# Kernel optimization log

Measured on AMD Instinct MI355X. Metric: run time of the kernel, lower is better.

## Reference

```python
import jax, jax.numpy as jnp
import numpy as np

V, E, H = 32000, 512, 1024  # vocab, embedding, hidden
B, T = 16, 256


def setup_inputs() -> dict:
    key = jax.random.key(0)
    ks = jax.random.split(key, 7)
    x = jax.random.randint(ks[0], (B, T), 0, V)
    emb = jax.random.normal(ks[1], (V, E), dtype=jnp.float32) * 0.02
    # Keras LSTMCell params: kernel [E,4H], recurrent_kernel [H,4H], bias [4H]
    kernel = jax.random.normal(ks[2], (E, 4 * H), dtype=jnp.float32) * (1.0 / np.sqrt(E))
    rec_kernel = jax.random.normal(ks[3], (H, 4 * H), dtype=jnp.float32) * (1.0 / np.sqrt(H))
    # unit_forget_bias: forget-gate bias initialized to 1 (gate order i,f,c,o)
    bias = jnp.concatenate([jnp.zeros(H), jnp.ones(H), jnp.zeros(2 * H)]).astype(jnp.float32)
    w_out = jax.random.normal(ks[4], (H, V), dtype=jnp.float32) * (1.0 / np.sqrt(H))
    b_out = jnp.zeros((V,), dtype=jnp.float32)
    return {"x": x, "emb": emb, "kernel": kernel, "rec_kernel": rec_kernel,
            "bias": bias, "w_out": w_out, "b_out": b_out}


def _lstm_scan(e, kernel, rec_kernel, bias):
    # e: [B, T, E] -> h_seq [B, T, H]
    Bsz = e.shape[0]
    Hs = rec_kernel.shape[0]
    # Precompute input projections for all timesteps (one big GEMM)
    zx = jnp.einsum('bte,ef->btf', e, kernel) + bias  # [B, T, 4H]
    zx_t = jnp.transpose(zx, (1, 0, 2))  # [T, B, 4H]

    def step(carry, zxt):
        h, c = carry
        z = zxt + h @ rec_kernel  # [B, 4H]
        i, f, g, o = jnp.split(z, 4, axis=-1)  # Keras gate order: i, f, c(g), o
        i = jax.nn.sigmoid(i)
        f = jax.nn.sigmoid(f)
        g = jnp.tanh(g)
        o = jax.nn.sigmoid(o)
        c = f * c + i * g
        h = o * jnp.tanh(c)
        return (h, c), h

    h0 = jnp.zeros((Bsz, Hs), dtype=e.dtype)
    c0 = jnp.zeros((Bsz, Hs), dtype=e.dtype)
    _, h_seq = jax.lax.scan(step, (h0, c0), zx_t)  # [T, B, H]
    return jnp.transpose(h_seq, (1, 0, 2))  # [B, T, H]


def reference(x, emb, kernel, rec_kernel, bias, w_out, b_out):
    e = emb[x]  # [B, T, E] embedding lookup
    h = _lstm_scan(e, kernel, rec_kernel, bias)  # [B, T, H]
    logits = jnp.einsum('bth,hv->btv', h, w_out) + b_out  # [B, T, V]
    return logits
```

## Files before the change

### kernel.cpp

```cpp
#include <hip/hip_runtime.h>
#include <cstdint>
#include <cstddef>

#define DEV __device__ __forceinline__

typedef __attribute__((ext_vector_type(4))) float f32x4;
typedef __attribute__((ext_vector_type(8))) short s16x8;
typedef __attribute__((ext_vector_type(4))) unsigned u32x4;

DEV uint16_t f2bf(float x){
  union { float f; uint32_t u; } v; v.f = x;
  uint32_t r = v.u + 0x7FFFu + ((v.u >> 16) & 1u);
  return (uint16_t)(r >> 16);
}
DEV float bf2f(uint16_t h){
  union { uint32_t u; float f; } v; v.u = ((uint32_t)h) << 16; return v.f;
}
DEV void split2(float x, uint16_t &hi, uint16_t &lo){
  hi = f2bf(x); lo = f2bf(x - bf2f(hi));
}

DEV f32x4 mfma16(s16x8 a, s16x8 b, f32x4 c){
  return __builtin_amdgcn_mfma_f32_16x16x32_bf16(a, b, c, 0, 0, 0);
}

DEV void g2l16(const void* g, void* l){
  __builtin_amdgcn_global_load_lds(
      (const __attribute__((address_space(1))) unsigned int*)g,
      (__attribute__((address_space(3))) unsigned int*)l, 16, 0, 0);
}

DEV s16x8 ldg_coh(const uint16_t* p){
  s16x8 r;
  asm volatile("global_load_dwordx4 %0, %1, off sc0 sc1" : "=v"(r) : "v"(p));
  return r;
}
DEV void stg_coh64(uint16_t* p, unsigned long long v){
  asm volatile("global_store_dwordx2 %0, %1, off sc0 sc1"
               :: "v"(p), "v"(v) : "memory");
}
DEV void stg_coh32(unsigned* p, unsigned v){
  asm volatile("global_store_dword %0, %1, off sc0 sc1"
               :: "v"(p), "v"(v) : "memory");
}
DEV u32x4 ldg_coh_u4(const unsigned* p){
  u32x4 r;
  asm volatile("global_load_dwordx4 %0, %1, off sc0 sc1\n\t"
               "s_waitcnt vmcnt(0)"
               : "=v"(r) : "v"(p) : "memory");
  return r;
}

__global__ void zero_u32(unsigned* __restrict__ p){ p[threadIdx.x] = 0u; }

__global__ __launch_bounds__(256) void gather_split(
    const int* __restrict__ x, const float* __restrict__ emb,
    uint16_t* __restrict__ ehi, uint16_t* __restrict__ elo){
  int idx = blockIdx.x * 256 + threadIdx.x;
  int r = idx >> 7, k4 = idx & 127;
  int row = x[r];
  float4 v = ((const float4*)(emb + (size_t)row * 512))[k4];
  ushort4 hi, lo;
  split2(v.x, hi.x, lo.x);
  split2(v.y, hi.y, lo.y);
  split2(v.z, hi.z, lo.z);
  split2(v.w, hi.w, lo.w);
  ((ushort4*)ehi)[idx] = hi;
  ((ushort4*)elo)[idx] = lo;
}

__global__ __launch_bounds__(256) void transpose_split(
    const float* __restrict__ in, uint16_t* __restrict__ ohi,
    uint16_t* __restrict__ olo, int R, int Cc){
  __shared__ float tile[32][33];
  const int tx = threadIdx.x & 31, ty = threadIdx.x >> 5;
  const int c0 = blockIdx.x << 5, r0 = blockIdx.y << 5;
  for (int i = 0; i < 32; i += 8)
    tile[ty + i][tx] = in[(size_t)(r0 + ty + i) * Cc + c0 + tx];
  __syncthreads();
  for (int i = 0; i < 32; i += 8){
    float v = tile[tx][ty + i];
    uint16_t hi, lo; split2(v, hi, lo);
    size_t o = (size_t)(c0 + ty + i) * R + r0 + tx;
    ohi[o] = hi; olo[o] = lo;
  }
}

__global__ __launch_bounds__(256) void pack_wr(
    const float* __restrict__ wr, uint16_t* __restrict__ phi, uint16_t* __restrict__ plo){
  int t = blockIdx.x * 256 + threadIdx.x;
  int lane = t & 63, kb = (t >> 6) & 31, ntile = t >> 11;
  int q = lane >> 4, ln = lane & 15;
  int n = ((ln >> 2) << 10) + (ntile << 2) + (ln & 3);
  int k0 = (kb << 5) + (q << 3);
  union { s16x8 v; uint16_t e[8]; } uh, ul;
  for (int j = 0; j < 8; j++)
    split2(wr[(size_t)(k0 + j) * 4096 + n], uh.e[j], ul.e[j]);
  ((s16x8*)phi)[t] = uh.v;
  ((s16x8*)plo)[t] = ul.v;
}

__global__ __launch_bounds__(256) void gemm_split(
    const uint16_t* __restrict__ Ahi, const uint16_t* __restrict__ Alo,
    const uint16_t* __restrict__ Bhi, const uint16_t* __restrict__ Blo,
    const float* __restrict__ bias, float* __restrict__ C,
    int Mm, int Nn, int Kk){
  __shared__ __attribute__((aligned(16))) uint16_t sAhi[2][128 * 32];
  __shared__ __attribute__((aligned(16))) uint16_t sAlo[2][128 * 32];
  __shared__ __attribute__((aligned(16))) uint16_t sBhi[2][128 * 32];
  __shared__ __attribute__((aligned(16))) uint16_t sBlo[2][128 * 32];

  const int tid = threadIdx.x;
  const int lane = tid & 63, wid = tid >> 6;
  const int wm = (wid & 1) * 64, wn = (wid >> 1) * 64;
  const int q = lane >> 4, lm = lane & 15;

  const int gm = Mm >> 7, gn = Nn >> 7;
  const int GROUP = 10;
  const int per = gm * GROUP;
  const int gi = blockIdx.x / per;
  const int rem = blockIdx.x - gi * per;
  const int n0g = gi * GROUP;
  int gw = gn - n0g; if (gw > GROUP) gw = GROUP;
  const int mt = rem / gw;
  const int nt = n0g + rem % gw;
  const int m0 = mt << 7, n0 = nt << 7;

  const int row0 = tid >> 2;
  const int csw  = (tid & 3) ^ ((row0 + (row0 >> 2)) & 3);
  const size_t aoff0 = (size_t)(m0 + row0) * Kk + csw * 8;
  const size_t aoff1 = (size_t)(m0 + row0 + 64) * Kk + csw * 8;
  const size_t boff0 = (size_t)(n0 + row0) * Kk + csw * 8;
  const size_t boff1 = (size_t)(n0 + row0 + 64) * Kk + csw * 8;

  const int qs8 = ((q ^ ((lm + (lm >> 2)) & 3)) * 8);

  auto STAGE = [&](int b, int ks){
    g2l16(Ahi + aoff0 + ks, sAhi[b] + tid * 8);
    g2l16(Ahi + aoff1 + ks, sAhi[b] + 2048 + tid * 8);
    g2l16(Alo + aoff0 + ks, sAlo[b] + tid * 8);
    g2l16(Alo + aoff1 + ks, sAlo[b] + 2048 + tid * 8);
    g2l16(Bhi + boff0 + ks, sBhi[b] + tid * 8);
    g2l16(Bhi + boff1 + ks, sBhi[b] + 2048 + tid * 8);
    g2l16(Blo + boff0 + ks, sBlo[b] + tid * 8);
    g2l16(Blo + boff1 + ks, sBlo[b] + 2048 + tid * 8);
  };

  f32x4 acc[4][4];
  for (int i = 0; i < 4; i++) for (int j = 0; j < 4; j++)
    acc[i][j] = (f32x4){0.f, 0.f, 0.f, 0.f};

  STAGE(0, 0);
  __syncthreads();

  int buf = 0;
  for (int ks = 0; ks < Kk; ks += 32){
    if (ks + 32 < Kk) STAGE(buf ^ 1, ks + 32);

    const uint16_t* pAh = sAhi[buf];
    const uint16_t* pAl = sAlo[buf];
    const uint16_t* pBh = sBhi[buf];
    const uint16_t* pBl = sBlo[buf];

    s16x8 bh[4], bl[4];
    for (int j = 0; j < 4; j++){
      bh[j] = *(const s16x8*)&pBh[(wn + j * 16 + lm) * 32 + qs8];
      bl[j] = *(const s16x8*)&pBl[(wn + j * 16 + lm) * 32 + qs8];
    }
    for (int i = 0; i < 4; i++){
      s16x8 ah = *(const s16x8*)&pAh[(wm + i * 16 + lm) * 32 + qs8];
      s16x8 al = *(const s16x8*)&pAl[(wm + i * 16 + lm) * 32 + qs8];
      for (int j = 0; j < 4; j++){
        acc[i][j] = mfma16(ah, bh[j], acc[i][j]);
        acc[i][j] = mfma16(ah, bl[j], acc[i][j]);
        acc[i][j] = mfma16(al, bh[j], acc[i][j]);
      }
    }
    __syncthreads();
    buf ^= 1;
  }

  for (int i = 0; i < 4; i++){
    const int rowg = m0 + wm + i * 16 + q * 4;
    for (int j = 0; j < 4; j++){
      const int colg = n0 + wn + j * 16 + lm;
      const float bv = bias[colg];
      for (int r = 0; r < 4; r++)
        C[(size_t)(rowg + r) * Nn + colg] = acc[i][j][r] + bv;
    }
  }
}

__global__ __launch_bounds__(256, 2) void lstm_fused(
    const uint16_t* __restrict__ wphi, const uint16_t* __restrict__ wplo,
    const float* __restrict__ zx,
    uint16_t* __restrict__ hseq_hi, uint16_t* __restrict__ hseq_lo,
    uint16_t* __restrict__ h0hi, uint16_t* __restrict__ h0lo,
    uint16_t* __restrict__ h1hi, uint16_t* __restrict__ h1lo,
    unsigned* __restrict__ flags, unsigned* __restrict__ epoch){
  __shared__ __attribute__((aligned(16))) uint16_t sWh[32 * 64 * 8];
  __shared__ __attribute__((aligned(16))) uint16_t sWl[32 * 64 * 8];
  __shared__ float zbuf[4][16][17];

  const int tid = threadIdx.x, lane = tid & 63, w = tid >> 6;
  const int q = lane >> 4, lm = lane & 15;
  const int blk = blockIdx.x;
  const int kq = w;
  const bool is_master = (blk == 0 && w == 0);

  {
    const uint16_t* gh = wphi + (size_t)blk * 16384;
    const uint16_t* gl = wplo + (size_t)blk * 16384;
#pragma unroll
    for (int i = 0; i < 8; i++){
      const int o = (i * 256 + tid) * 8;
      g2l16(gh + o, sWh + o);
      g2l16(gl + o, sWl + o);
    }
    asm volatile("s_waitcnt vmcnt(0)" ::: "memory");
  }
  __syncthreads();

  const int aoffbase = lm * 1024 + kq * 256 + q * 8;
  const int boffbase = kq * 8 * 512 + lane * 8;

  const int tb = tid >> 2, ccin = tid & 3;
  const int thcol = blk * 4 + ccin;
  const unsigned* epoll = epoch + (blk & 7) * 32;
  float cval = 0.f;

  for (int t = 0; t < 256; t++){
    float zr0 = 0.f, zr1 = 0.f, zr2 = 0.f, zr3 = 0.f;
    if (tid < 64){
      const float* zr = zx + ((size_t)tb * 256 + t) * 4096 + thcol;
      zr0 = zr[0]; zr1 = zr[1024]; zr2 = zr[2048]; zr3 = zr[3072];
    }

    f32x4 a0 = (f32x4){0.f,0.f,0.f,0.f};
    f32x4 a1 = (f32x4){0.f,0.f,0.f,0.f};
    f32x4 a2 = (f32x4){0.f,0.f,0.f,0.f};
    if (t > 0){
      if (!is_master){
        const unsigned gen = (unsigned)t;
        for (;;){
          unsigned v;
          asm volatile("global_load_dword %0, %1, off sc0 sc1\n\t"
                       "s_waitcnt vmcnt(0)"
                       : "=v"(v) : "v"(epoll) : "memory");
          if (v >= gen) break;
          __builtin_amdgcn_s_sleep(1);
        }
      }
      __builtin_amdgcn_sched_barrier(0);

      const uint16_t* hih = (t & 1) ? h1hi : h0hi;
      const uint16_t* hil = (t & 1) ? h1lo : h0lo;
      const uint16_t* ah_p = hih + aoffbase;
      const uint16_t* al_p = hil + aoffbase;
      s16x8 Ah[8], Al[8];
#pragma unroll
      for (int kb = 0; kb < 8; kb++){
        Ah[kb] = ldg_coh(ah_p + kb * 32);
        Al[kb] = ldg_coh(al_p + kb * 32);
      }
      asm volatile("s_waitcnt vmcnt(0)" ::: "memory");
      __builtin_amdgcn_sched_barrier(0);
#pragma unroll
      for (int kb = 0; kb < 8; kb++){
        s16x8 bh = *(const s16x8*)&sWh[boffbase + kb * 512];
        s16x8 bl = *(const s16x8*)&sWl[boffbase + kb * 512];
        a0 = mfma16(Ah[kb], bh, a0);
        a1 = mfma16(Ah[kb], bl, a1);
        a2 = mfma16(Al[kb], bh, a2);
      }
    }
    f32x4 acc = a0 + a1 + a2;

#pragma unroll
    for (int r = 0; r < 4; r++)
      zbuf[w][q * 4 + r][lm] = acc[r];
    __syncthreads();

    if (tid < 64){
      const size_t rrow = (size_t)tb * 256 + t;
      float z0 = zbuf[0][tb][0 * 4 + ccin] + zbuf[1][tb][0 * 4 + ccin]
               + zbuf[2][tb][0 * 4 + ccin] + zbuf[3][tb][0 * 4 + ccin] + zr0;
      float z1 = zbuf[0][tb][1 * 4 + ccin] + zbuf[1][tb][1 * 4 + ccin]
               + zbuf[2][tb][1 * 4 + ccin] + zbuf[3][tb][1 * 4 + ccin] + zr1;
      float z2 = zbuf[0][tb][2 * 4 + ccin] + zbuf[1][tb][2 * 4 + ccin]
               + zbuf[2][tb][2 * 4 + ccin] + zbuf[3][tb][2 * 4 + ccin] + zr2;
      float z3 = zbuf[0][tb][3 * 4 + ccin] + zbuf[1][tb][3 * 4 + ccin]
               + zbuf[2][tb][3 * 4 + ccin] + zbuf[3][tb][3 * 4 + ccin] + zr3;
      float ig = 1.f / (1.f + __expf(-z0));
      float fg = 1.f / (1.f + __expf(-z1));
      float gg = 1.f - 2.f / (__expf(2.f * z2) + 1.f);
      float og = 1.f / (1.f + __expf(-z3));
      cval = fg * cval + ig * gg;
      float h = og * (1.f - 2.f / (__expf(2.f * cval) + 1.f));
      uint16_t hh, hl; split2(h, hh, hl);

      unsigned pk = (unsigned)hh | ((unsigned)hl << 16);
      unsigned p1 = __shfl_down(pk, 1);
      unsigned p2 = __shfl_down(pk, 2);
      unsigned p3 = __shfl_down(pk, 3);
      if (ccin == 0){
        union { unsigned u32[2]; unsigned long long u64; } vhi, vlo;
        vhi.u32[0] = (pk & 0xFFFFu) | ((p1 & 0xFFFFu) << 16);
        vhi.u32[1] = (p2 & 0xFFFFu) | ((p3 & 0xFFFFu) << 16);
        vlo.u32[0] = (pk >> 16) | (p1 & 0xFFFF0000u);
        vlo.u32[1] = (p2 >> 16) | (p3 & 0xFFFF0000u);
        uint16_t* ohh = ((t & 1) ? h0hi : h1hi) + tb * 1024 + blk * 4;
        uint16_t* ohl = ((t & 1) ? h0lo : h1lo) + tb * 1024 + blk * 4;
        stg_coh64(ohh, vhi.u64);
        stg_coh64(ohl, vlo.u64);
      }
      asm volatile("s_waitcnt vmcnt(0)" ::: "memory");
      if (tid == 0)
        stg_coh32(flags + blk, (unsigned)(t + 1));
      hseq_hi[rrow * 1024 + thcol] = hh;
      hseq_lo[rrow * 1024 + thcol] = hl;
    }

    if (is_master && t < 255){
      const unsigned gen = (unsigned)(t + 1);
      for (;;){
        u32x4 f = ldg_coh_u4(flags + lane * 4);
        if (__all(f.x >= gen && f.y >= gen && f.z >= gen && f.w >= gen)) break;
        __builtin_amdgcn_s_sleep(1);
      }
      if (lane < 8)
        stg_coh32(epoch + lane * 32, gen);
    }
  }
}

extern "C" void kernel_launch(void* const* d_in, const int* in_sizes, int n_in,
                              void* d_out, int out_size, void* d_ws, size_t ws_size,
                              hipStream_t stream){
  (void)in_sizes; (void)n_in; (void)out_size; (void)ws_size;
  const int*   x    = (const int*)d_in[0];
  const float* emb  = (const float*)d_in[1];
  const float* wk   = (const float*)d_in[2];
  const float* wr   = (const float*)d_in[3];
  const float* bias = (const float*)d_in[4];
  const float* wo   = (const float*)d_in[5];
  const float* bo   = (const float*)d_in[6];
  float* out = (float*)d_out;

  char* w = (char*)d_ws;
  float*    zx    = (float*)w;    w += (size_t)4096 * 4096 * 4;
  uint16_t* ehi   = (uint16_t*)w; w += (size_t)4096 * 512 * 2;
  uint16_t* elo   = (uint16_t*)w; w += (size_t)4096 * 512 * 2;
  uint16_t* kthi  = (uint16_t*)w; w += (size_t)4096 * 512 * 2;
  uint16_t* ktlo  = (uint16_t*)w; w += (size_t)4096 * 512 * 2;
  uint16_t* wphi  = (uint16_t*)w; w += (size_t)1024 * 4096 * 2;
  uint16_t* wplo  = (uint16_t*)w; w += (size_t)1024 * 4096 * 2;
  uint16_t* wothi = (uint16_t*)w; w += (size_t)32000 * 1024 * 2;
  uint16_t* wotlo = (uint16_t*)w; w += (size_t)32000 * 1024 * 2;
  uint16_t* hshi  = (uint16_t*)w; w += (size_t)4096 * 1024 * 2;
  uint16_t* hslo  = (uint16_t*)w; w += (size_t)4096 * 1024 * 2;
  uint16_t* h0hi  = (uint16_t*)w; w += (size_t)16 * 1024 * 2;
  uint16_t* h0lo  = (uint16_t*)w; w += (size_t)16 * 1024 * 2;
  uint16_t* h1hi  = (uint16_t*)w; w += (size_t)16 * 1024 * 2;
  uint16_t* h1lo  = (uint16_t*)w; w += (size_t)16 * 1024 * 2;
  unsigned* flags = (unsigned*)w; w += 256 * 4;
  unsigned* epoch = (unsigned*)w; w += 256 * 4;

  zero_u32<<<1, 512, 0, stream>>>(flags);
  gather_split<<<2048, 256, 0, stream>>>(x, emb, ehi, elo);
  transpose_split<<<dim3(128, 16), 256, 0, stream>>>(wk, kthi, ktlo, 512, 4096);
  pack_wr<<<2048, 256, 0, stream>>>(wr, wphi, wplo);
  transpose_split<<<dim3(1000, 32), 256, 0, stream>>>(wo, wothi, wotlo, 1024, 32000);

  gemm_split<<<1024, 256, 0, stream>>>(ehi, elo, kthi, ktlo, bias, zx,
                                       4096, 4096, 512);

  {
    void* kargs[] = {
      (void*)&wphi, (void*)&wplo, (void*)&zx,
      (void*)&hshi, (void*)&hslo,
      (void*)&h0hi, (void*)&h0lo, (void*)&h1hi, (void*)&h1lo,
      (void*)&flags, (void*)&epoch
    };
    (void)hipLaunchCooperativeKernel((void*)lstm_fused, dim3(256), dim3(256),
                                     kargs, 0, stream);
  }

  gemm_split<<<8000, 256, 0, stream>>>(hshi, hslo, wothi, wotlo, bo, out,
                                       4096, 32000, 1024);
}
```

Measured before the change: 2.818 ms.

## Enlarge split-bf16 GEMM tiles to 256x256 with 8 waves and explicit pipelining

The split-precision GEMM goes from 128x128 tiles with 4 waves to 256x256 tiles with 512 threads. Each wave now computes a 128x64 sub-tile. The K loop prefetches two stages ahead using explicit vmcnt waits, raw s_barrier calls and setprio around the MFMA phases. The aim is to raise arithmetic intensity and keep MFMA units busy in the large output-projection GEMM. In exchange it uses much more LDS and registers, runs one block per CU, and leaves fewer blocks for the small input-projection GEMM.

New measurement: 2.874 ms. 1.02x slower.

```diff
diff --git a/kernel.cpp b/kernel.cpp
--- a/kernel.cpp
+++ b/kernel.cpp
@@ -100,23 +100,23 @@
   ((s16x8*)plo)[t] = ul.v;
 }
 
-__global__ __launch_bounds__(256) void gemm_split(
+__global__ __launch_bounds__(512, 1) void gemm_split(
     const uint16_t* __restrict__ Ahi, const uint16_t* __restrict__ Alo,
     const uint16_t* __restrict__ Bhi, const uint16_t* __restrict__ Blo,
     const float* __restrict__ bias, float* __restrict__ C,
     int Mm, int Nn, int Kk){
-  __shared__ __attribute__((aligned(16))) uint16_t sAhi[2][128 * 32];
-  __shared__ __attribute__((aligned(16))) uint16_t sAlo[2][128 * 32];
-  __shared__ __attribute__((aligned(16))) uint16_t sBhi[2][128 * 32];
-  __shared__ __attribute__((aligned(16))) uint16_t sBlo[2][128 * 32];
+  __shared__ __attribute__((aligned(16))) uint16_t sAh[2][8192];
+  __shared__ __attribute__((aligned(16))) uint16_t sAl[2][8192];
+  __shared__ __attribute__((aligned(16))) uint16_t sBh[2][8192];
+  __shared__ __attribute__((aligned(16))) uint16_t sBl[2][8192];
 
   const int tid = threadIdx.x;
   const int lane = tid & 63, wid = tid >> 6;
-  const int wm = (wid & 1) * 64, wn = (wid >> 1) * 64;
+  const int wm = (wid & 1) * 128, wn = (wid >> 1) * 64;
   const int q = lane >> 4, lm = lane & 15;
 
-  const int gm = Mm >> 7, gn = Nn >> 7;
-  const int GROUP = 10;
+  const int gm = Mm >> 8, gn = Nn >> 8;
+  const int GROUP = 8;
   const int per = gm * GROUP;
   const int gi = blockIdx.x / per;
   const int rem = blockIdx.x - gi * per;
@@ -124,63 +124,89 @@
   int gw = gn - n0g; if (gw > GROUP) gw = GROUP;
   const int mt = rem / gw;
   const int nt = n0g + rem % gw;
-  const int m0 = mt << 7, n0 = nt << 7;
+  const int m0 = mt << 8, n0 = nt << 8;
 
   const int row0 = tid >> 2;
   const int csw  = (tid & 3) ^ ((row0 + (row0 >> 2)) & 3);
-  const size_t aoff0 = (size_t)(m0 + row0) * Kk + csw * 8;
-  const size_t aoff1 = (size_t)(m0 + row0 + 64) * Kk + csw * 8;
-  const size_t boff0 = (size_t)(n0 + row0) * Kk + csw * 8;
-  const size_t boff1 = (size_t)(n0 + row0 + 64) * Kk + csw * 8;
+  const size_t aoffA0 = (size_t)(m0 + row0) * Kk + csw * 8;
+  const size_t aoffA1 = (size_t)(m0 + row0 + 128) * Kk + csw * 8;
+  const size_t aoffB0 = (size_t)(n0 + row0) * Kk + csw * 8;
+  const size_t aoffB1 = (size_t)(n0 + row0 + 128) * Kk + csw * 8;
 
   const int qs8 = ((q ^ ((lm + (lm >> 2)) & 3)) * 8);
 
   auto STAGE = [&](int b, int ks){
-    g2l16(Ahi + aoff0 + ks, sAhi[b] + tid * 8);
-    g2l16(Ahi + aoff1 + ks, sAhi[b] + 2048 + tid * 8);
-    g2l16(Alo + aoff0 + ks, sAlo[b] + tid * 8);
-    g2l16(Alo + aoff1 + ks, sAlo[b] + 2048 + tid * 8);
-    g2l16(Bhi + boff0 + ks, sBhi[b] + tid * 8);
-    g2l16(Bhi + boff1 + ks, sBhi[b] + 2048 + tid * 8);
-    g2l16(Blo + boff0 + ks, sBlo[b] + tid * 8);
-    g2l16(Blo + boff1 + ks, sBlo[b] + 2048 + tid * 8);
+    g2l16(Ahi + aoffA0 + ks, &sAh[b][tid * 8]);
+    g2l16(Ahi + aoffA1 + ks, &sAh[b][(tid + 512) * 8]);
+    g2l16(Alo + aoffA0 + ks, &sAl[b][tid * 8]);
+    g2l16(Alo + aoffA1 + ks, &sAl[b][(tid + 512) * 8]);
+    g2l16(Bhi + aoffB0 + ks, &sBh[b][tid * 8]);
+    g2l16(Bhi + aoffB1 + ks, &sBh[b][(tid + 512) * 8]);
+    g2l16(Blo + aoffB0 + ks, &sBl[b][tid * 8]);
+    g2l16(Blo + aoffB1 + ks, &sBl[b][(tid + 512) * 8]);
   };
 
-  f32x4 acc[4][4];
-  for (int i = 0; i < 4; i++) for (int j = 0; j < 4; j++)
-    acc[i][j] = (f32x4){0.f, 0.f, 0.f, 0.f};
-
+  f32x4 acc[8][4];
+#pragma unroll
+  for (int i = 0; i < 8; i++)
+#pragma unroll
+    for (int j = 0; j < 4; j++)
+      acc[i][j] = (f32x4){0.f, 0.f, 0.f, 0.f};
+
+  const int ns = Kk >> 5;
   STAGE(0, 0);
-  __syncthreads();
-
-  int buf = 0;
-  for (int ks = 0; ks < Kk; ks += 32){
-    if (ks + 32 < Kk) STAGE(buf ^ 1, ks + 32);
-
-    const uint16_t* pAh = sAhi[buf];
-    const uint16_t* pAl = sAlo[buf];
-    const uint16_t* pBh = sBhi[buf];
-    const uint16_t* pBl = sBlo[buf];
-
-    s16x8 bh[4], bl[4];
-    for (int j = 0; j < 4; j++){
-      bh[j] = *(const s16x8*)&pBh[(wn + j * 16 + lm) * 32 + qs8];
-      bl[j] = *(const s16x8*)&pBl[(wn + j * 16 + lm) * 32 + qs8];
-    }
-    for (int i = 0; i < 4; i++){
-      s16x8 ah = *(const s16x8*)&pAh[(wm + i * 16 + lm) * 32 + qs8];
-      s16x8 al = *(const s16x8*)&pAl[(wm + i * 16 + lm) * 32 + qs8];
-      for (int j = 0; j < 4; j++){
-        acc[i][j] = mfma16(ah, bh[j], acc[i][j]);
-        acc[i][j] = mfma16(ah, bl[j], acc[i][j]);
-        acc[i][j] = mfma16(al, bh[j], acc[i][j]);
-      }
-    }
-    __syncthreads();
-    buf ^= 1;
-  }
-
-  for (int i = 0; i < 4; i++){
+  if (ns > 1) STAGE(1, 32);
+
+  for (int it = 0; it < ns; ++it){
+    const int ks = it << 5;
+    const int buf = it & 1;
+
+    if (it + 1 < ns) asm volatile("s_waitcnt vmcnt(8)" ::: "memory");
+    else             asm volatile("s_waitcnt vmcnt(0)" ::: "memory");
+    __builtin_amdgcn_sched_barrier(0);
+    __builtin_amdgcn_s_barrier();
+    __builtin_amdgcn_sched_barrier(0);
+
+#pragma unroll
+    for (int ph = 0; ph < 4; ++ph){
+      const int mq = ph & 1, nq = ph >> 1;
+      s16x8 ah[4], al[4], bh[2], bl[2];
+#pragma unroll
+      for (int ii = 0; ii < 4; ii++){
+        const int row = wm + (mq * 4 + ii) * 16 + lm;
+        ah[ii] = *(const s16x8*)&sAh[buf][row * 32 + qs8];
+        al[ii] = *(const s16x8*)&sAl[buf][row * 32 + qs8];
+      }
+#pragma unroll
+      for (int jj = 0; jj < 2; jj++){
+        const int row = wn + (nq * 2 + jj) * 16 + lm;
+        bh[jj] = *(const s16x8*)&sBh[buf][row * 32 + qs8];
+        bl[jj] = *(const s16x8*)&sBl[buf][row * 32 + qs8];
+      }
+      if (ph == 3){
+        asm volatile("s_waitcnt lgkmcnt(0)" ::: "memory");
+        __builtin_amdgcn_sched_barrier(0);
+        __builtin_amdgcn_s_barrier();
+        if (ks + 64 < Kk) STAGE(buf, ks + 64);
+      }
+      __builtin_amdgcn_s_setprio(1);
+#pragma unroll
+      for (int ii = 0; ii < 4; ii++){
+        const int ai = mq * 4 + ii;
+#pragma unroll
+        for (int jj = 0; jj < 2; jj++){
+          const int bj = nq * 2 + jj;
+          acc[ai][bj] = mfma16(ah[ii], bh[jj], acc[ai][bj]);
+          acc[ai][bj] = mfma16(ah[ii], bl[jj], acc[ai][bj]);
+          acc[ai][bj] = mfma16(al[ii], bh[jj], acc[ai][bj]);
+        }
+      }
+      __builtin_amdgcn_s_setprio(0);
+      __builtin_amdgcn_s_barrier();
+    }
+  }
+
+  for (int i = 0; i < 8; i++){
     const int rowg = m0 + wm + i * 16 + q * 4;
     for (int j = 0; j < 4; j++){
       const int colg = n0 + wn + j * 16 + lm;
@@ -372,8 +398,8 @@
   pack_wr<<<2048, 256, 0, stream>>>(wr, wphi, wplo);
   transpose_split<<<dim3(1000, 32), 256, 0, stream>>>(wo, wothi, wotlo, 1024, 32000);
 
-  gemm_split<<<1024, 256, 0, stream>>>(ehi, elo, kthi, ktlo, bias, zx,
-                                       4096, 4096, 512);
+  gemm_split<<<256, 512, 0, stream>>>(ehi, elo, kthi, ktlo, bias, zx,
+                                      4096, 4096, 512);
 
   {
     void* kargs[] = {
@@ -386,6 +412,6 @@
                                      kargs, 0, stream);
   }
 
-  gemm_split<<<8000, 256, 0, stream>>>(hshi, hslo, wothi, wotlo, bo, out,
+  gemm_split<<<2000, 512, 0, stream>>>(hshi, hslo, wothi, wotlo, bo, out,
                                        4096, 32000, 1024);
 }
```

## Overlap output projection GEMM with LSTM recurrence in one cooperative kernel

Applied to the files above, without the earlier changes.

Launches 512 cooperative blocks. The first 256 run the LSTM recurrence, and the rest compute output-logit GEMM tiles as soon as the epoch counter shows the needed timesteps are finished. Hidden states are written in time-major (rotated) order so that each 128-row tile covers 8 complete timesteps, and the epilogue permutes rows back to batch-major order. This hides the large vocab GEMM behind the latency-bound recurrence. The cost is that the GEMM blocks share the GPU with the recurrence blocks and may slow its critical path. A fallback to separate launches is kept in case the 512-block cooperative launch fails.

Result: faster. 2.300 ms (-18.4%).

```diff
diff --git a/kernel.cpp b/kernel.cpp
--- a/kernel.cpp
+++ b/kernel.cpp
@@ -49,6 +49,13 @@
                "s_waitcnt vmcnt(0)"
                : "=v"(r) : "v"(p) : "memory");
   return r;
+}
+DEV unsigned ldg_coh_u1(const unsigned* p){
+  unsigned v;
+  asm volatile("global_load_dword %0, %1, off sc0 sc1\n\t"
+               "s_waitcnt vmcnt(0)"
+               : "=v"(v) : "v"(p) : "memory");
+  return v;
 }
 
 __global__ void zero_u32(unsigned* __restrict__ p){ p[threadIdx.x] = 0u; }
@@ -104,7 +111,7 @@
     const uint16_t* __restrict__ Ahi, const uint16_t* __restrict__ Alo,
     const uint16_t* __restrict__ Bhi, const uint16_t* __restrict__ Blo,
     const float* __restrict__ bias, float* __restrict__ C,
-    int Mm, int Nn, int Kk){
+    int Mm, int Nn, int Kk, int rowperm){
   __shared__ __attribute__((aligned(16))) uint16_t sAhi[2][128 * 32];
   __shared__ __attribute__((aligned(16))) uint16_t sAlo[2][128 * 32];
   __shared__ __attribute__((aligned(16))) uint16_t sBhi[2][128 * 32];
@@ -185,26 +192,132 @@
     for (int j = 0; j < 4; j++){
       const int colg = n0 + wn + j * 16 + lm;
       const float bv = bias[colg];
-      for (int r = 0; r < 4; r++)
-        C[(size_t)(rowg + r) * Nn + colg] = acc[i][j][r] + bv;
-    }
-  }
-}
+      for (int r = 0; r < 4; r++){
+        int rg = rowg + r;
+        if (rowperm) rg = ((rg & 15) << 8) | (rg >> 4);
+        C[(size_t)rg * Nn + colg] = acc[i][j][r] + bv;
+      }
+    }
+  }
+}
+
+struct SMemRec {
+  uint16_t Wh[32 * 64 * 8];
+  uint16_t Wl[32 * 64 * 8];
+  float zbuf[4][16][17];
+};
+struct SMemGw {
+  uint16_t Ah[2][4096];
+  uint16_t Al[2][4096];
+  uint16_t Bh[2][4096];
+  uint16_t Bl[2][4096];
+};
+union SMemU { SMemRec rec; SMemGw gw; };
 
 __global__ __launch_bounds__(256, 2) void lstm_fused(
     const uint16_t* __restrict__ wphi, const uint16_t* __restrict__ wplo,
     const float* __restrict__ zx,
-    uint16_t* __restrict__ hseq_hi, uint16_t* __restrict__ hseq_lo,
+    uint16_t* __restrict__ hrot_hi, uint16_t* __restrict__ hrot_lo,
     uint16_t* __restrict__ h0hi, uint16_t* __restrict__ h0lo,
     uint16_t* __restrict__ h1hi, uint16_t* __restrict__ h1lo,
-    unsigned* __restrict__ flags, unsigned* __restrict__ epoch){
-  __shared__ __attribute__((aligned(16))) uint16_t sWh[32 * 64 * 8];
-  __shared__ __attribute__((aligned(16))) uint16_t sWl[32 * 64 * 8];
-  __shared__ float zbuf[4][16][17];
+    unsigned* __restrict__ flags, unsigned* __restrict__ epoch,
+    const uint16_t* __restrict__ wothi, const uint16_t* __restrict__ wotlo,
+    const float* __restrict__ bo, float* __restrict__ out){
+  __shared__ __attribute__((aligned(16))) SMemU sm;
 
   const int tid = threadIdx.x, lane = tid & 63, w = tid >> 6;
+  const int blk = blockIdx.x;
+
+  if (blk >= 256){
+    const int wb = blk - 256;
+    const int wid = tid >> 6;
+    const int wm = (wid & 1) * 64, wn = (wid >> 1) * 64;
+    const int q = lane >> 4, lm = lane & 15;
+    const int row0 = tid >> 2;
+    const int csw = (tid & 3) ^ ((row0 + (row0 >> 2)) & 3);
+    const int qs8 = ((q ^ ((lm + (lm >> 2)) & 3)) * 8);
+    const unsigned* ep = epoch + (wb & 7) * 32;
+
+    for (int idx = wb; idx < 8000; idx += 256){
+      const int mt = idx / 250, nt = idx - mt * 250;
+      const unsigned need = (unsigned)(mt * 8 + 8);
+      for (;;){
+        if (ldg_coh_u1(ep) >= need) break;
+        __builtin_amdgcn_s_sleep(2);
+      }
+      __builtin_amdgcn_sched_barrier(0);
+
+      const int m0 = mt << 7, n0 = nt << 7;
+      const size_t aoff0 = (size_t)(m0 + row0) * 1024 + csw * 8;
+      const size_t aoff1 = (size_t)(m0 + row0 + 64) * 1024 + csw * 8;
+      const size_t boff0 = (size_t)(n0 + row0) * 1024 + csw * 8;
+      const size_t boff1 = (size_t)(n0 + row0 + 64) * 1024 + csw * 8;
+
+      auto STAGEW = [&](int b, int ks){
+        g2l16(hrot_hi + aoff0 + ks, &sm.gw.Ah[b][tid * 8]);
+        g2l16(hrot_hi + aoff1 + ks, &sm.gw.Ah[b][2048 + tid * 8]);
+        g2l16(hrot_lo + aoff0 + ks, &sm.gw.Al[b][tid * 8]);
+        g2l16(hrot_lo + aoff1 + ks, &sm.gw.Al[b][2048 + tid * 8]);
+        g2l16(wothi + boff0 + ks, &sm.gw.Bh[b][tid * 8]);
+        g2l16(wothi + boff1 + ks, &sm.gw.Bh[b][2048 + tid * 8]);
+        g2l16(wotlo + boff0 + ks, &sm.gw.Bl[b][tid * 8]);
+        g2l16(wotlo + boff1 + ks, &sm.gw.Bl[b][2048 + tid * 8]);
+      };
+
+      f32x4 acc[4][4];
+#pragma unroll
+      for (int i = 0; i < 4; i++)
+#pragma unroll
+        for (int j = 0; j < 4; j++)
+          acc[i][j] = (f32x4){0.f, 0.f, 0.f, 0.f};
+
+      STAGEW(0, 0);
+      __syncthreads();
+      int buf = 0;
+      for (int ks = 0; ks < 1024; ks += 32){
+        if (ks + 32 < 1024) STAGEW(buf ^ 1, ks + 32);
+        const uint16_t* pAh = sm.gw.Ah[buf];
+        const uint16_t* pAl = sm.gw.Al[buf];
+        const uint16_t* pBh = sm.gw.Bh[buf];
+        const uint16_t* pBl = sm.gw.Bl[buf];
+        s16x8 bh[4], bl[4];
+#pragma unroll
+        for (int j = 0; j < 4; j++){
+          bh[j] = *(const s16x8*)&pBh[(wn + j * 16 + lm) * 32 + qs8];
+          bl[j] = *(const s16x8*)&pBl[(wn + j * 16 + lm) * 32 + qs8];
+        }
+#pragma unroll
+        for (int i = 0; i < 4; i++){
+          s16x8 ah = *(const s16x8*)&pAh[(wm + i * 16 + lm) * 32 + qs8];
+          s16x8 al = *(const s16x8*)&pAl[(wm + i * 16 + lm) * 32 + qs8];
+#pragma unroll
+          for (int j = 0; j < 4; j++){
+            acc[i][j] = mfma16(ah, bh[j], acc[i][j]);
+            acc[i][j] = mfma16(ah, bl[j], acc[i][j]);
+            acc[i][j] = mfma16(al, bh[j], acc[i][j]);
+          }
+        }
+        __syncthreads();
+        buf ^= 1;
+      }
+
+      for (int i = 0; i < 4; i++){
+        const int rowg = m0 + wm + i * 16 + q * 4;
+        for (int j = 0; j < 4; j++){
+          const int colg = n0 + wn + j * 16 + lm;
+          const float bv = bo[colg];
+          for (int r = 0; r < 4; r++){
+            int rg = rowg + r;
+            rg = ((rg & 15) << 8) | (rg >> 4);
+            out[(size_t)rg * 32000 + colg] = acc[i][j][r] + bv;
+          }
+        }
+      }
+    }
+    return;
+  }
+
   const int q = lane >> 4, lm = lane & 15;
-  const int blk = blockIdx.x;
   const int kq = w;
   const bool is_master = (blk == 0 && w == 0);
 
@@ -214,8 +327,8 @@
 #pragma unroll
     for (int i = 0; i < 8; i++){
       const int o = (i * 256 + tid) * 8;
-      g2l16(gh + o, sWh + o);
-      g2l16(gl + o, sWl + o);
+      g2l16(gh + o, sm.rec.Wh + o);
+      g2l16(gl + o, sm.rec.Wl + o);
     }
     asm volatile("s_waitcnt vmcnt(0)" ::: "memory");
   }
@@ -243,11 +356,7 @@
       if (!is_master){
         const unsigned gen = (unsigned)t;
         for (;;){
-          unsigned v;
-          asm volatile("global_load_dword %0, %1, off sc0 sc1\n\t"
-                       "s_waitcnt vmcnt(0)"
-                       : "=v"(v) : "v"(epoll) : "memory");
-          if (v >= gen) break;
+          if (ldg_coh_u1(epoll) >= gen) break;
           __builtin_amdgcn_s_sleep(1);
         }
       }
@@ -267,8 +376,8 @@
       __builtin_amdgcn_sched_barrier(0);
 #pragma unroll
       for (int kb = 0; kb < 8; kb++){
-        s16x8 bh = *(const s16x8*)&sWh[boffbase + kb * 512];
-        s16x8 bl = *(const s16x8*)&sWl[boffbase + kb * 512];
+        s16x8 bh = *(const s16x8*)&sm.rec.Wh[boffbase + kb * 512];
+        s16x8 bl = *(const s16x8*)&sm.rec.Wl[boffbase + kb * 512];
         a0 = mfma16(Ah[kb], bh, a0);
         a1 = mfma16(Ah[kb], bl, a1);
         a2 = mfma16(Al[kb], bh, a2);
@@ -278,19 +387,18 @@
 
 #pragma unroll
     for (int r = 0; r < 4; r++)
-      zbuf[w][q * 4 + r][lm] = acc[r];
+      sm.rec.zbuf[w][q * 4 + r][lm] = acc[r];
     __syncthreads();
 
     if (tid < 64){
-      const size_t rrow = (size_t)tb * 256 + t;
-      float z0 = zbuf[0][tb][0 * 4 + ccin] + zbuf[1][tb][0 * 4 + ccin]
-               + zbuf[2][tb][0 * 4 + ccin] + zbuf[3][tb][0 * 4 + ccin] + zr0;
-      float z1 = zbuf[0][tb][1 * 4 + ccin] + zbuf[1][tb][1 * 4 + ccin]
-               + zbuf[2][tb][1 * 4 + ccin] + zbuf[3][tb][1 * 4 + ccin] + zr1;
-      float z2 = zbuf[0][tb][2 * 4 + ccin] + zbuf[1][tb][2 * 4 + ccin]
-               + zbuf[2][tb][2 * 4 + ccin] + zbuf[3][tb][2 * 4 + ccin] + zr2;
-      float z3 = zbuf[0][tb][3 * 4 + ccin] + zbuf[1][tb][3 * 4 + ccin]
-               + zbuf[2][tb][3 * 4 + ccin] + zbuf[3][tb][3 * 4 + ccin] + zr3;
+      float z0 = sm.rec.zbuf[0][tb][0 * 4 + ccin] + sm.rec.zbuf[1][tb][0 * 4 + ccin]
+               + sm.rec.zbuf[2][tb][0 * 4 + ccin] + sm.rec.zbuf[3][tb][0 * 4 + ccin] + zr0;
+      float z1 = sm.rec.zbuf[0][tb][1 * 4 + ccin] + sm.rec.zbuf[1][tb][1 * 4 + ccin]
+               + sm.rec.zbuf[2][tb][1 * 4 + ccin] + sm.rec.zbuf[3][tb][1 * 4 + ccin] + zr1;
+      float z2 = sm.rec.zbuf[0][tb][2 * 4 + ccin] + sm.rec.zbuf[1][tb][2 * 4 + ccin]
+               + sm.rec.zbuf[2][tb][2 * 4 + ccin] + sm.rec.zbuf[3][tb][2 * 4 + ccin] + zr2;
+      float z3 = sm.rec.zbuf[0][tb][3 * 4 + ccin] + sm.rec.zbuf[1][tb][3 * 4 + ccin]
+               + sm.rec.zbuf[2][tb][3 * 4 + ccin] + sm.rec.zbuf[3][tb][3 * 4 + ccin] + zr3;
       float ig = 1.f / (1.f + __expf(-z0));
       float fg = 1.f / (1.f + __expf(-z1));
       float gg = 1.f - 2.f / (__expf(2.f * z2) + 1.f);
@@ -313,12 +421,14 @@
         uint16_t* ohl = ((t & 1) ? h0lo : h1lo) + tb * 1024 + blk * 4;
         stg_coh64(ohh, vhi.u64);
         stg_coh64(ohl, vlo.u64);
+        uint16_t* rh = hrot_hi + ((size_t)(t * 16 + tb)) * 1024 + blk * 4;
+        uint16_t* rl = hrot_lo + ((size_t)(t * 16 + tb)) * 1024 + blk * 4;
+        stg_coh64(rh, vhi.u64);
+        stg_coh64(rl, vlo.u64);
       }
       asm volatile("s_waitcnt vmcnt(0)" ::: "memory");
       if (tid == 0)
         stg_coh32(flags + blk, (unsigned)(t + 1));
-      hseq_hi[rrow * 1024 + thcol] = hh;
-      hseq_lo[rrow * 1024 + thcol] = hl;
     }
 
     if (is_master && t < 255){
@@ -331,6 +441,17 @@
       if (lane < 8)
         stg_coh32(epoch + lane * 32, gen);
     }
+  }
+
+  if (is_master){
+    const unsigned gen = 256u;
+    for (;;){
+      u32x4 f = ldg_coh_u4(flags + lane * 4);
+      if (__all(f.x >= gen && f.y >= gen && f.z >= gen && f.w >= gen)) break;
+      __builtin_amdgcn_s_sleep(1);
+    }
+    if (lane < 8)
+      stg_coh32(epoch + lane * 32, gen);
   }
 }
 
@@ -357,8 +478,8 @@
   uint16_t* wplo  = (uint16_t*)w; w += (size_t)1024 * 4096 * 2;
   uint16_t* wothi = (uint16_t*)w; w += (size_t)32000 * 1024 * 2;
   uint16_t* wotlo = (uint16_t*)w; w += (size_t)32000 * 1024 * 2;
-  uint16_t* hshi  = (uint16_t*)w; w += (size_t)4096 * 1024 * 2;
-  uint16_t* hslo  = (uint16_t*)w; w += (size_t)4096 * 1024 * 2;
+  uint16_t* hroth = (uint16_t*)w; w += (size_t)4096 * 1024 * 2;
+  uint16_t* hrotl = (uint16_t*)w; w += (size_t)4096 * 1024 * 2;
   uint16_t* h0hi  = (uint16_t*)w; w += (size_t)16 * 1024 * 2;
   uint16_t* h0lo  = (uint16_t*)w; w += (size_t)16 * 1024 * 2;
   uint16_t* h1hi  = (uint16_t*)w; w += (size_t)16 * 1024 * 2;
@@ -373,19 +494,23 @@
   transpose_split<<<dim3(1000, 32), 256, 0, stream>>>(wo, wothi, wotlo, 1024, 32000);
 
   gemm_split<<<1024, 256, 0, stream>>>(ehi, elo, kthi, ktlo, bias, zx,
-                                       4096, 4096, 512);
+                                       4096, 4096, 512, 0);
 
   {
     void* kargs[] = {
       (void*)&wphi, (void*)&wplo, (void*)&zx,
-      (void*)&hshi, (void*)&hslo,
+      (void*)&hroth, (void*)&hrotl,
       (void*)&h0hi, (void*)&h0lo, (void*)&h1hi, (void*)&h1lo,
-      (void*)&flags, (void*)&epoch
+      (void*)&flags, (void*)&epoch,
+      (void*)&wothi, (void*)&wotlo, (void*)&bo, (void*)&out
     };
-    (void)hipLaunchCooperativeKernel((void*)lstm_fused, dim3(256), dim3(256),
-                                     kargs, 0, stream);
-  }
-
-  gemm_split<<<8000, 256, 0, stream>>>(hshi, hslo, wothi, wotlo, bo, out,
-                                       4096, 32000, 1024);
-}
+    hipError_t ce = hipLaunchCooperativeKernel((void*)lstm_fused, dim3(512),
+                                               dim3(256), kargs, 0, stream);
+    if (ce != hipSuccess){
+      (void)hipLaunchCooperativeKernel((void*)lstm_fused, dim3(256),
+                                       dim3(256), kargs, 0, stream);
+      gemm_split<<<8000, 256, 0, stream>>>(hroth, hrotl, wothi, wotlo, bo, out,
+                                           4096, 32000, 1024, 1);
+    }
+  }
+}
```
